# Performance work log

Hardware: AMD Instinct MI355X
Metric: run time of the kernel (lower is better)

The kernel has to match this reference:

```python
import jax, jax.numpy as jnp
import numpy as np

B, C, H, W = 2, 512, 64, 64
NUM_HEADS = 8
HEAD_DIM = C // NUM_HEADS


def setup_inputs() -> dict:
    key = jax.random.key(0)
    ks = jax.random.split(key, 6)
    s = 1.0 / np.sqrt(C)
    return {
        "x": jax.random.normal(ks[0], (B, C, H, W), dtype=jnp.float32),
        "w_qkv": jax.random.normal(ks[1], (3 * C, C), dtype=jnp.float32) * s,
        "b_qkv": jax.random.normal(ks[2], (3 * C,), dtype=jnp.float32) * 0.01,
        "w_out": jax.random.normal(ks[3], (C, C), dtype=jnp.float32) * s,
        "b_out": jax.random.normal(ks[4], (C,), dtype=jnp.float32) * 0.01,
        "gamma": jax.random.normal(ks[5], (1,), dtype=jnp.float32) * 0.1,
    }


def reference(x, w_qkv, b_qkv, w_out, b_out, gamma):
    b, c, h, w = x.shape
    n = h * w
    nh, hd = NUM_HEADS, HEAD_DIM
    # 1x1 conv QKV projection == per-pixel linear
    qkv = jnp.einsum('oc,bchw->bohw', w_qkv, x) + b_qkv[None, :, None, None]
    qkv = qkv.reshape(b, 3, nh, hd, n)  # [B,3,nh,hd,N]
    q = qkv[:, 0].transpose(0, 1, 3, 2)  # [B,nh,N,hd]
    k = qkv[:, 1]                        # [B,nh,hd,N]
    v = qkv[:, 2].transpose(0, 1, 3, 2)  # [B,nh,N,hd]
    scale = hd ** -0.5
    attn = jnp.einsum('bhnd,bhdm->bhnm', q, k) * scale  # [B,nh,N,N]
    attn = jax.nn.softmax(attn, axis=-1)
    out = jnp.einsum('bhnm,bhmd->bhnd', attn, v)  # [B,nh,N,hd]
    out = out.transpose(0, 1, 3, 2).reshape(b, c, h, w)  # [B,C,H,W]
    out = jnp.einsum('oc,bchw->bohw', w_out, out) + b_out[None, :, None, None]
    return gamma[0] * out + x
```

## Files before the change

### kernel.cpp

```cpp
#include <hip/hip_runtime.h>
#include <hip/hip_bf16.h>

typedef __bf16 bf16_t;
typedef __bf16 bf16x8 __attribute__((ext_vector_type(8)));
typedef __bf16 bf16x4 __attribute__((ext_vector_type(4)));
typedef float floatx4 __attribute__((ext_vector_type(4)));
typedef float f32x16 __attribute__((ext_vector_type(16)));

#define MFMA_BF16(a, b, c) __builtin_amdgcn_mfma_f32_16x16x32_bf16((a), (b), (c), 0, 0, 0)
#define MFMA32(a, b, c) __builtin_amdgcn_mfma_f32_32x32x16_bf16((a), (b), (c), 0, 0, 0)

static constexpr int CB = 512;
static constexpr int NB = 4096;

__device__ __forceinline__ unsigned cvtpk_bf16(float lo, float hi_) {
  unsigned r;
  asm("v_cvt_pk_bf16_f32 %0, %1, %2" : "=v"(r) : "v"(lo), "v"(hi_));
  return r;
}
__device__ __forceinline__ void plswap(unsigned& x, unsigned& y) {
  asm volatile("v_permlane32_swap_b32 %0, %1" : "+v"(x), "+v"(y));
}
__device__ __forceinline__ float exp2_fast(float x) {
  float r;
  asm("v_exp_f32 %0, %1" : "=v"(r) : "v"(x));
  return r;
}

#define GLOAD_LDS16(gsrc, ldst)                                              \
  __builtin_amdgcn_global_load_lds(                                          \
      (const __attribute__((address_space(1))) void*)(gsrc),                 \
      (__attribute__((address_space(3))) void*)(ldst), 16, 0, 0)

__global__ __launch_bounds__(256) void k_cvtw(const float* __restrict__ w_qkv,
                                              const float* __restrict__ w_out,
                                              bf16_t* __restrict__ Wb,
                                              bf16_t* __restrict__ Wo) {
  const int idx = (blockIdx.x * 256 + threadIdx.x) * 8;
  const float* src;
  bf16_t* dst;
  if (idx < 786432) { src = w_qkv + idx; dst = Wb + idx; }
  else              { src = w_out + (idx - 786432); dst = Wo + (idx - 786432); }
  const float4 a = *reinterpret_cast<const float4*>(src);
  const float4 b = *reinterpret_cast<const float4*>(src + 4);
  union { unsigned u[4]; bf16x8 v; } o;
  o.u[0] = cvtpk_bf16(a.x, a.y);
  o.u[1] = cvtpk_bf16(a.z, a.w);
  o.u[2] = cvtpk_bf16(b.x, b.y);
  o.u[3] = cvtpk_bf16(b.z, b.w);
  *reinterpret_cast<bf16x8*>(dst) = o.v;
}

__global__ __launch_bounds__(256) void k_transpose(const float* __restrict__ x,
                                                   bf16_t* __restrict__ xT) {
  __shared__ __align__(16) bf16_t T[64 * 72];
  const int t = threadIdx.x;
  const int b = blockIdx.z, c0 = blockIdx.y * 64, n0 = blockIdx.x * 64;
  {
    const int cl = t >> 4, nl = (t & 15) * 4;
#pragma unroll
    for (int p = 0; p < 4; ++p) {
      const int c = cl + p * 16;
      const float4 v = *reinterpret_cast<const float4*>(
          x + ((size_t)(b * CB + c0 + c) * NB) + n0 + nl);
      T[(nl + 0) * 72 + c] = (bf16_t)v.x;
      T[(nl + 1) * 72 + c] = (bf16_t)v.y;
      T[(nl + 2) * 72 + c] = (bf16_t)v.z;
      T[(nl + 3) * 72 + c] = (bf16_t)v.w;
    }
  }
  __syncthreads();
  {
    const int nr = t >> 2, ch = t & 3;
    bf16_t* op = xT + ((size_t)(b * NB + n0 + nr) * CB) + c0;
#pragma unroll
    for (int p = 0; p < 2; ++p) {
      bf16x8 v = *reinterpret_cast<const bf16x8*>(&T[nr * 72 + ch * 8 + p * 32]);
      *reinterpret_cast<bf16x8*>(op + ch * 8 + p * 32) = v;
    }
  }
}

__global__ __launch_bounds__(256, 2) void k_qkv(const bf16_t* __restrict__ Wb,
                                                const float* __restrict__ bias,
                                                const bf16_t* __restrict__ xT,
                                                bf16_t* __restrict__ Qb,
                                                bf16_t* __restrict__ Kb,
                                                bf16_t* __restrict__ Vb) {
  __shared__ __align__(16) bf16_t As[2][128 * 64];
  __shared__ __align__(16) bf16_t Bs[2][128 * 64];
  const int t = threadIdx.x, lane = t & 63, w = t >> 6;
  const int g = lane >> 4, c = lane & 15;
  const int wm = w >> 1, wn = w & 1;
  const int o0 = blockIdx.x * 128, n0 = blockIdx.y * 128;
  const int b = blockIdx.z;

  floatx4 acc[4][4] = {};

  const int srow = t >> 3;
  const int gch = (t & 7) ^ (srow & 7);
  const bf16_t* asrc = Wb + (size_t)(o0 + srow) * CB + gch * 8;
  const bf16_t* bsrc = xT + ((size_t)(b * NB + n0 + srow)) * CB + gch * 8;

#define QSTAGE(kt_, bufi)                                                     \
  do {                                                                        \
    _Pragma("unroll")                                                         \
    for (int p = 0; p < 4; ++p) {                                             \
      GLOAD_LDS16(asrc + (size_t)p * 32 * CB + (kt_),                         \
                  &As[(bufi)][w * 512 + p * 2048]);                           \
      GLOAD_LDS16(bsrc + (size_t)p * 32 * CB + (kt_),                         \
                  &Bs[(bufi)][w * 512 + p * 2048]);                           \
    }                                                                         \
  } while (0)

  int cho[2];
  cho[0] = (g ^ (c & 7)) * 8;
  cho[1] = ((4 + g) ^ (c & 7)) * 8;

  QSTAGE(0, 0);
  asm volatile("s_waitcnt vmcnt(0)" ::: "memory");
  __builtin_amdgcn_s_barrier();
  __builtin_amdgcn_sched_barrier(0);

  int buf = 0;
  for (int s = 0; s < 8; ++s) {
    if (s < 7) QSTAGE((s + 1) * 64, buf ^ 1);
#pragma unroll
    for (int ksub = 0; ksub < 2; ++ksub) {
      bf16x8 af[4], bfr[4];
#pragma unroll
      for (int i = 0; i < 4; ++i)
        af[i] = *reinterpret_cast<const bf16x8*>(
            &As[buf][(wm * 64 + i * 16 + c) * 64 + cho[ksub]]);
#pragma unroll
      for (int j = 0; j < 4; ++j)
        bfr[j] = *reinterpret_cast<const bf16x8*>(
            &Bs[buf][(wn * 64 + j * 16 + c) * 64 + cho[ksub]]);
#pragma unroll
      for (int i = 0; i < 4; ++i)
#pragma unroll
        for (int j = 0; j < 4; ++j)
          acc[i][j] = MFMA_BF16(af[i], bfr[j], acc[i][j]);
    }
    if (s < 7) {
      asm volatile("s_waitcnt vmcnt(0) lgkmcnt(0)" ::: "memory");
      __builtin_amdgcn_s_barrier();
      __builtin_amdgcn_sched_barrier(0);
      buf ^= 1;
    }
  }
#undef QSTAGE

  const int which = o0 >> 9;
#pragma unroll
  for (int i = 0; i < 4; ++i) {
    const int ob = o0 + wm * 64 + i * 16 + 4 * g;
    float bias4[4];
#pragma unroll
    for (int r = 0; r < 4; ++r) bias4[r] = bias[ob + r];
    const int h = (ob >> 6) & 7;
    const int d0 = ob & 63;
#pragma unroll
    for (int j = 0; j < 4; ++j) {
      const int n = n0 + wn * 64 + j * 16 + c;
      if (which == 2) {
        bf16_t* vp = Vb + (size_t)(b * 8 + h) * 64 * NB + n;
#pragma unroll
        for (int r = 0; r < 4; ++r)
          vp[(size_t)(d0 + r) * NB] = (bf16_t)(acc[i][j][r] + bias4[r]);
      } else {
        bf16_t* qp = (which == 0 ? Qb : Kb) + ((size_t)(b * 8 + h) * NB + n) * 64 + d0;
        bf16x4 pk;
#pragma unroll
        for (int r = 0; r < 4; ++r) pk[r] = (bf16_t)(acc[i][j][r] + bias4[r]);
        *reinterpret_cast<bf16x4*>(qp) = pk;
      }
    }
  }
}

__global__ __launch_bounds__(256, 2) void k_attn(const bf16_t* __restrict__ Qb,
                                                 const bf16_t* __restrict__ Kb,
                                                 const bf16_t* __restrict__ Vb,
                                                 bf16_t* __restrict__ P0,
                                                 bf16_t* __restrict__ P1,
                                                 float* __restrict__ lsum) {
  __shared__ __align__(16) bf16_t Kl[2][2][4096];
  __shared__ __align__(16) bf16_t Vl[2][2][4096];
  const int t = threadIdx.x, lane = t & 63, w = t >> 6;
  const int q31 = lane & 31, hi = lane >> 5;

  const int bid = blockIdx.x;
  const int xcd = bid & 7, j = bid >> 3;
  const int bh = xcd * 2 + (j >> 6);
  const int rest = j & 63;
  const int qt = rest >> 1, half = rest & 1;
  const int q0 = qt * 128 + w * 32;
  const int kvbase = half * 2048;

  const size_t base = (size_t)bh * NB * 64;
  const bf16_t* Qp = Qb + base;
  const bf16_t* Kp = Kb + base;
  const bf16_t* Vp = Vb + base;
  bf16_t* Op = (half ? P1 : P0) + base;

  const float SC = 0.125f * 1.44269504088896340736f;
  const float FM = 8.0f;

  bf16x8 qf[4];
#pragma unroll
  for (int ks = 0; ks < 4; ++ks) {
    bf16x8 q = *reinterpret_cast<const bf16x8*>(Qp + (size_t)(q0 + q31) * 64 + ks * 16 + hi * 8);
#pragma unroll
    for (int e = 0; e < 8; ++e) q[e] = (bf16_t)((float)q[e] * SC);
    qf[ks] = q;
  }

  bf16x8 ones;
#pragma unroll
  for (int e = 0; e < 8; ++e) ones[e] = (bf16_t)1.0f;

  const int srow0 = t >> 3, srow1 = srow0 + 32;
  const int sc0 = ((t & 7) ^ (srow0 & 7)) * 8;
  const int sc1 = ((t & 7) ^ (srow1 & 7)) * 8;
  const bf16_t* ksrc0 = Kp + (size_t)(kvbase + srow0) * 64 + sc0;
  const bf16_t* ksrc1 = Kp + (size_t)(kvbase + srow1) * 64 + sc1;
  const bf16_t* vsrc0 = Vp + (size_t)srow0 * NB + kvbase + sc0;
  const bf16_t* vsrc1 = Vp + (size_t)srow1 * NB + kvbase + sc1;

#define STAGE128(ss, bufi)                                                    \
  do {                                                                        \
    const size_t ko_ = (size_t)(ss) * 8192;                                   \
    const int vo_ = (ss) * 128;                                               \
    bf16_t* kd0_ = &Kl[(bufi)][0][0];                                         \
    bf16_t* kd1_ = &Kl[(bufi)][1][0];                                         \
    bf16_t* vd0_ = &Vl[(bufi)][0][0];                                         \
    bf16_t* vd1_ = &Vl[(bufi)][1][0];                                         \
    GLOAD_LDS16(ksrc0 + ko_, kd0_ + w * 512);                                 \
    GLOAD_LDS16(ksrc1 + ko_, kd0_ + 2048 + w * 512);                          \
    GLOAD_LDS16(ksrc0 + ko_ + 4096, kd1_ + w * 512);                          \
    GLOAD_LDS16(ksrc1 + ko_ + 4096, kd1_ + 2048 + w * 512);                   \
    GLOAD_LDS16(vsrc0 + vo_, vd0_ + w * 512);                                 \
    GLOAD_LDS16(vsrc1 + vo_, vd0_ + 2048 + w * 512);                          \
    GLOAD_LDS16(vsrc0 + vo_ + 64, vd1_ + w * 512);                            \
    GLOAD_LDS16(vsrc1 + vo_ + 64, vd1_ + 2048 + w * 512);                     \
  } while (0)

  int c16r[4];
#pragma unroll
  for (int ks = 0; ks < 4; ++ks) c16r[ks] = ((ks * 2 + hi) ^ (q31 & 7)) * 8;

  f32x16 O0 = {}, O1 = {}, lacc = {};
  f32x16 NEGM;
#pragma unroll
  for (int r = 0; r < 16; ++r) NEGM[r] = -FM;

  STAGE128(0, 0);
  asm volatile("s_waitcnt vmcnt(0)" ::: "memory");
  __builtin_amdgcn_s_barrier();
  __builtin_amdgcn_sched_barrier(0);

  int buf = 0;
  for (int s = 0; s < 16; ++s) {
    if (s < 15) STAGE128(s + 1, buf ^ 1);
#pragma unroll
    for (int sub = 0; sub < 2; ++sub) {
      const bf16_t* Kbuf = &Kl[buf][sub][0];
      const bf16_t* Vbuf = &Vl[buf][sub][0];
      f32x16 st0 = NEGM, st1 = NEGM;
      __builtin_amdgcn_s_setprio(1);
#pragma unroll
      for (int ks = 0; ks < 4; ++ks) {
        bf16x8 kf0 = *reinterpret_cast<const bf16x8*>(&Kbuf[q31 * 64 + c16r[ks]]);
        bf16x8 kf1 = *reinterpret_cast<const bf16x8*>(&Kbuf[(32 + q31) * 64 + c16r[ks]]);
        st0 = MFMA32(kf0, qf[ks], st0);
        st1 = MFMA32(kf1, qf[ks], st1);
      }
      __builtin_amdgcn_s_setprio(0);

#pragma unroll
      for (int r = 0; r < 16; ++r) st0[r] = exp2_fast(st0[r]);
#pragma unroll
      for (int r = 0; r < 16; ++r) st1[r] = exp2_fast(st1[r]);

      __builtin_amdgcn_s_setprio(1);
#pragma unroll
      for (int ks = 0; ks < 4; ++ks) {
        const f32x16& P = (ks < 2) ? st0 : st1;
        const int rb = (ks & 1) * 8;
        unsigned x0 = cvtpk_bf16(P[rb + 0], P[rb + 1]);
        unsigned y0 = cvtpk_bf16(P[rb + 4], P[rb + 5]);
        unsigned x1 = cvtpk_bf16(P[rb + 2], P[rb + 3]);
        unsigned y1 = cvtpk_bf16(P[rb + 6], P[rb + 7]);
        plswap(x0, y0);
        plswap(x1, y1);
        union { unsigned u[4]; bf16x8 v; } pa;
        pa.u[0] = x0; pa.u[1] = x1; pa.u[2] = y0; pa.u[3] = y1;
        bf16x8 vf0 = *reinterpret_cast<const bf16x8*>(&Vbuf[q31 * 64 + c16r[ks]]);
        bf16x8 vf1 = *reinterpret_cast<const bf16x8*>(&Vbuf[(32 + q31) * 64 + c16r[ks]]);
        O0 = MFMA32(pa.v, vf0, O0);
        O1 = MFMA32(pa.v, vf1, O1);
        lacc = MFMA32(pa.v, ones, lacc);
      }
      __builtin_amdgcn_s_setprio(0);
    }
    if (s < 15) {
      asm volatile("s_waitcnt vmcnt(0) lgkmcnt(0)" ::: "memory");
      __builtin_amdgcn_s_barrier();
      __builtin_amdgcn_sched_barrier(0);
    }
    buf ^= 1;
  }
#undef STAGE128

#pragma unroll
  for (int r = 0; r < 16; ++r) {
    const int n = q0 + (r & 3) + 8 * (r >> 2) + 4 * hi;
    bf16_t* op = Op + ((size_t)n) * 64 + q31;
    op[0]  = (bf16_t)O0[r];
    op[32] = (bf16_t)O1[r];
  }
  if (q31 == 0) {
    float* lp = lsum + (size_t)(half * 16 + bh) * NB;
#pragma unroll
    for (int r = 0; r < 16; ++r) {
      const int row = (r & 3) + 8 * (r >> 2) + 4 * hi;
      lp[q0 + row] = lacc[r];
    }
  }
}

__global__ __launch_bounds__(256) void k_out(const bf16_t* __restrict__ Wo,
                                             const float* __restrict__ bias,
                                             const bf16_t* __restrict__ P0,
                                             const bf16_t* __restrict__ P1,
                                             const float* __restrict__ lsum,
                                             const float* __restrict__ x,
                                             const float* __restrict__ gamma,
                                             float* __restrict__ y) {
  __shared__ __align__(16) bf16_t As[128 * 64];
  __shared__ __align__(16) bf16_t Bs[128 * 40];
  const int t = threadIdx.x;
  const int lane = t & 63, w = t >> 6;
  const int g = lane >> 4, c = lane & 15;
  const int wm = w >> 1, wn = w & 1;
  const int o0 = blockIdx.x * 128, n0 = blockIdx.y * 128;
  const int b = blockIdx.z;

  floatx4 acc[4][4] = {};

  const int srow = t >> 3;
  const int gch = (t & 7) ^ (srow & 7);
  const bf16_t* asrc = Wo + (size_t)(o0 + srow) * CB + gch * 8;

  for (int kt = 0; kt < CB; kt += 32) {
    if ((kt & 63) == 0) {
#pragma unroll
      for (int p = 0; p < 4; ++p)
        GLOAD_LDS16(asrc + (size_t)p * 32 * CB + kt, &As[w * 512 + p * 2048]);
    }
    {
      const int row = t >> 2, ch = t & 3;
      const int cc = kt + ch * 8;
      const int h = cc >> 6, d = cc & 63;
#pragma unroll
      for (int p = 0; p < 2; ++p) {
        const int r = row + p * 64;
        const int n = n0 + r;
        const size_t li = (size_t)(b * 8 + h) * NB + n;
        const size_t idx = li * 64 + d;
        const bf16x8 oa = *reinterpret_cast<const bf16x8*>(P0 + idx);
        const bf16x8 ob = *reinterpret_cast<const bf16x8*>(P1 + idx);
        const float rl = 1.0f / (lsum[li] + lsum[li + 16 * NB]);
        bf16x8 o;
#pragma unroll
        for (int e = 0; e < 8; ++e)
          o[e] = (bf16_t)(((float)oa[e] + (float)ob[e]) * rl);
        *reinterpret_cast<bf16x8*>(&Bs[r * 40 + ch * 8]) = o;
      }
    }
    __syncthreads();
    const int ksub = (kt >> 5) & 1;
    const int acho = ((ksub * 4 + g) ^ (c & 7)) * 8;
    bf16x8 af[4], bfr[4];
#pragma unroll
    for (int i = 0; i < 4; ++i)
      af[i] = *reinterpret_cast<const bf16x8*>(&As[(wm * 64 + i * 16 + c) * 64 + acho]);
#pragma unroll
    for (int j = 0; j < 4; ++j)
      bfr[j] = *reinterpret_cast<const bf16x8*>(&Bs[(wn * 64 + j * 16 + c) * 40 + g * 8]);
#pragma unroll
    for (int i = 0; i < 4; ++i)
#pragma unroll
      for (int j = 0; j < 4; ++j)
        acc[i][j] = MFMA_BF16(af[i], bfr[j], acc[i][j]);
    __syncthreads();
  }

  const float gm = gamma[0];
#pragma unroll
  for (int i = 0; i < 4; ++i) {
    const int ob = o0 + wm * 64 + i * 16 + 4 * g;
    float bias4[4];
#pragma unroll
    for (int r = 0; r < 4; ++r) bias4[r] = bias[ob + r];
#pragma unroll
    for (int j = 0; j < 4; ++j) {
      const int n = n0 + wn * 64 + j * 16 + c;
      const float* xp = x + ((size_t)(b * CB + ob) * NB) + n;
      float* yp = y + ((size_t)(b * CB + ob) * NB) + n;
#pragma unroll
      for (int r = 0; r < 4; ++r)
        yp[(size_t)r * NB] = gm * (acc[i][j][r] + bias4[r]) + xp[(size_t)r * NB];
    }
  }
}

extern "C" void kernel_launch(void* const* d_in, const int* in_sizes, int n_in,
                              void* d_out, int out_size, void* d_ws, size_t ws_size,
                              hipStream_t stream) {
  const float* x      = (const float*)d_in[0];
  const float* w_qkv  = (const float*)d_in[1];
  const float* b_qkv  = (const float*)d_in[2];
  const float* w_out  = (const float*)d_in[3];
  const float* b_out  = (const float*)d_in[4];
  const float* gamma  = (const float*)d_in[5];
  float* y = (float*)d_out;

  const size_t CH = 4194304;
  bf16_t* Wp = (bf16_t*)d_ws;
  bf16_t* Qb = Wp;
  bf16_t* Kb = Wp + CH;
  bf16_t* Vb = Wp + 2 * CH;
  bf16_t* P1 = Wp + 3 * CH;
  bf16_t* xT = Wp + 4 * CH;
  bf16_t* P0 = Wp + 4 * CH;
  bf16_t* Wb = Wp + 5 * CH;
  bf16_t* Wo = Wb + 786432;
  float*  lsum = (float*)(Wo + 262144);

  k_cvtw<<<dim3(512), 256, 0, stream>>>(w_qkv, w_out, Wb, Wo);
  k_transpose<<<dim3(64, 8, 2), 256, 0, stream>>>(x, xT);
  k_qkv<<<dim3(12, 32, 2), 256, 0, stream>>>(Wb, b_qkv, xT, Qb, Kb, Vb);
  k_attn<<<dim3(1024), 256, 0, stream>>>(Qb, Kb, Vb, P0, P1, lsum);
  k_out<<<dim3(4, 32, 2), 256, 0, stream>>>(Wo, b_out, P0, P1, lsum, x, gamma, y);
}
```

Before: 148.4 us.

## Compute softmax row sums with VALU dot2 and merge prep kernels

Replaces the extra MFMA that multiplied P by a ones vector to get softmax denominators with bf16 dot2 VALU accumulations per lane, combined across the two lane halves with a shuffle. This removes a third of the MFMA work in the attention inner loop at the cost of a few VALU ops. Also merges the weight conversion and input transpose kernels into a single launch to save launch overhead.

```diff
diff --git a/kernel.cpp b/kernel.cpp
--- a/kernel.cpp
+++ b/kernel.cpp
@@ -26,35 +26,40 @@
   asm("v_exp_f32 %0, %1" : "=v"(r) : "v"(x));
   return r;
 }
+__device__ __forceinline__ void dot2_bf16(float& d, unsigned a, unsigned b) {
+  asm("v_dot2_f32_bf16 %0, %1, %2, %0" : "+v"(d) : "v"(a), "v"(b));
+}
 
 #define GLOAD_LDS16(gsrc, ldst)                                              \
   __builtin_amdgcn_global_load_lds(                                          \
       (const __attribute__((address_space(1))) void*)(gsrc),                 \
       (__attribute__((address_space(3))) void*)(ldst), 16, 0, 0)
 
-__global__ __launch_bounds__(256) void k_cvtw(const float* __restrict__ w_qkv,
+__global__ __launch_bounds__(256) void k_prep(const float* __restrict__ x,
+                                              bf16_t* __restrict__ xT,
+                                              const float* __restrict__ w_qkv,
                                               const float* __restrict__ w_out,
                                               bf16_t* __restrict__ Wb,
                                               bf16_t* __restrict__ Wo) {
-  const int idx = (blockIdx.x * 256 + threadIdx.x) * 8;
-  const float* src;
-  bf16_t* dst;
-  if (idx < 786432) { src = w_qkv + idx; dst = Wb + idx; }
-  else              { src = w_out + (idx - 786432); dst = Wo + (idx - 786432); }
-  const float4 a = *reinterpret_cast<const float4*>(src);
-  const float4 b = *reinterpret_cast<const float4*>(src + 4);
-  union { unsigned u[4]; bf16x8 v; } o;
-  o.u[0] = cvtpk_bf16(a.x, a.y);
-  o.u[1] = cvtpk_bf16(a.z, a.w);
-  o.u[2] = cvtpk_bf16(b.x, b.y);
-  o.u[3] = cvtpk_bf16(b.z, b.w);
-  *reinterpret_cast<bf16x8*>(dst) = o.v;
-}
-
-__global__ __launch_bounds__(256) void k_transpose(const float* __restrict__ x,
-                                                   bf16_t* __restrict__ xT) {
+  const int t = threadIdx.x;
+  if (blockIdx.y >= 8) {
+    const int widx = (blockIdx.z * 4 + (blockIdx.y - 8)) * 64 + blockIdx.x;
+    const int idx = (widx * 256 + t) * 8;
+    const float* src;
+    bf16_t* dst;
+    if (idx < 786432) { src = w_qkv + idx; dst = Wb + idx; }
+    else              { src = w_out + (idx - 786432); dst = Wo + (idx - 786432); }
+    const float4 a = *reinterpret_cast<const float4*>(src);
+    const float4 b = *reinterpret_cast<const float4*>(src + 4);
+    union { unsigned u[4]; bf16x8 v; } o;
+    o.u[0] = cvtpk_bf16(a.x, a.y);
+    o.u[1] = cvtpk_bf16(a.z, a.w);
+    o.u[2] = cvtpk_bf16(b.x, b.y);
+    o.u[3] = cvtpk_bf16(b.z, b.w);
+    *reinterpret_cast<bf16x8*>(dst) = o.v;
+    return;
+  }
   __shared__ __align__(16) bf16_t T[64 * 72];
-  const int t = threadIdx.x;
   const int b = blockIdx.z, c0 = blockIdx.y * 64, n0 = blockIdx.x * 64;
   {
     const int cl = t >> 4, nl = (t & 15) * 4;
@@ -216,9 +221,7 @@
     qf[ks] = q;
   }
 
-  bf16x8 ones;
-#pragma unroll
-  for (int e = 0; e < 8; ++e) ones[e] = (bf16_t)1.0f;
+  const unsigned ONE2 = 0x3F803F80u;
 
   const int srow0 = t >> 3, srow1 = srow0 + 32;
   const int sc0 = ((t & 7) ^ (srow0 & 7)) * 8;
@@ -250,7 +253,8 @@
 #pragma unroll
   for (int ks = 0; ks < 4; ++ks) c16r[ks] = ((ks * 2 + hi) ^ (q31 & 7)) * 8;
 
-  f32x16 O0 = {}, O1 = {}, lacc = {};
+  f32x16 O0 = {}, O1 = {};
+  float lp0 = 0.f, lp1 = 0.f, lp2 = 0.f, lp3 = 0.f;
   f32x16 NEGM;
 #pragma unroll
   for (int r = 0; r < 16; ++r) NEGM[r] = -FM;
@@ -296,11 +300,14 @@
         plswap(x1, y1);
         union { unsigned u[4]; bf16x8 v; } pa;
         pa.u[0] = x0; pa.u[1] = x1; pa.u[2] = y0; pa.u[3] = y1;
+        dot2_bf16(lp0, pa.u[0], ONE2);
+        dot2_bf16(lp1, pa.u[1], ONE2);
+        dot2_bf16(lp2, pa.u[2], ONE2);
+        dot2_bf16(lp3, pa.u[3], ONE2);
         bf16x8 vf0 = *reinterpret_cast<const bf16x8*>(&Vbuf[q31 * 64 + c16r[ks]]);
         bf16x8 vf1 = *reinterpret_cast<const bf16x8*>(&Vbuf[(32 + q31) * 64 + c16r[ks]]);
         O0 = MFMA32(pa.v, vf0, O0);
         O1 = MFMA32(pa.v, vf1, O1);
-        lacc = MFMA32(pa.v, ones, lacc);
       }
       __builtin_amdgcn_s_setprio(0);
     }
@@ -320,12 +327,12 @@
     op[0]  = (bf16_t)O0[r];
     op[32] = (bf16_t)O1[r];
   }
-  if (q31 == 0) {
-    float* lp = lsum + (size_t)(half * 16 + bh) * NB;
-#pragma unroll
-    for (int r = 0; r < 16; ++r) {
-      const int row = (r & 3) + 8 * (r >> 2) + 4 * hi;
-      lp[q0 + row] = lacc[r];
+  {
+    float lfin = (lp0 + lp1) + (lp2 + lp3);
+    lfin += __shfl_xor(lfin, 32);
+    if (hi == 0) {
+      float* lp_ = lsum + (size_t)(half * 16 + bh) * NB;
+      lp_[q0 + q31] = lfin;
     }
   }
 }
@@ -439,8 +446,7 @@
   bf16_t* Wo = Wb + 786432;
   float*  lsum = (float*)(Wo + 262144);
 
-  k_cvtw<<<dim3(512), 256, 0, stream>>>(w_qkv, w_out, Wb, Wo);
-  k_transpose<<<dim3(64, 8, 2), 256, 0, stream>>>(x, xT);
+  k_prep<<<dim3(64, 12, 2), 256, 0, stream>>>(x, xT, w_qkv, w_out, Wb, Wo);
   k_qkv<<<dim3(12, 32, 2), 256, 0, stream>>>(Wb, b_qkv, xT, Qb, Kb, Vb);
   k_attn<<<dim3(1024), 256, 0, stream>>>(Qb, Kb, Vb, P0, P1, lsum);
   k_out<<<dim3(4, 32, 2), 256, 0, stream>>>(Wo, b_out, P0, P1, lsum, x, gamma, y);
```

Measured after the change: 136.5 us. 1.09x faster.
